# Optimization experiments

Measured on AMD Instinct MI355X. Metric: run time of the kernel, lower is better.

The kernel has to match this reference:

```python
import jax, jax.numpy as jnp
import numpy as np

BETA = 0.25  # commitment_weight


def _conv(x, w, b=None, stride=1, pad=0):
    y = jax.lax.conv_general_dilated(x, w, (stride, stride), ((pad, pad), (pad, pad)),
                                     dimension_numbers=('NCHW', 'OIHW', 'NCHW'))
    return y if b is None else y + b[None, :, None, None]


def _convT(x, w, b):
    # PyTorch ConvTranspose2d(kernel=4, stride=2, padding=1); w stored as (in, out, 4, 4)
    wf = jnp.flip(w, (2, 3)).transpose(1, 0, 2, 3)  # -> OIHW, spatially flipped
    y = jax.lax.conv_general_dilated(x, wf, (1, 1), ((2, 2), (2, 2)), lhs_dilation=(2, 2),
                                     dimension_numbers=('NCHW', 'OIHW', 'NCHW'))
    return y + b[None, :, None, None]


def _res(x, wa, wb):
    # ResidualLayer: x + conv1x1(relu(conv3x3(x))) , both convs bias-free
    return x + _conv(jax.nn.relu(_conv(x, wa, pad=1)), wb)


def _lrelu(x):
    return jax.nn.leaky_relu(x, 0.01)


def setup_inputs() -> dict:
    key = jax.random.key(0)
    ks = iter(jax.random.split(key, 32))
    def p(shape, s=0.05):
        return jax.random.normal(next(ks), shape, jnp.float32) * s
    inp = {
        'inputs': jax.random.normal(next(ks), (16, 4, 256, 256), jnp.float32),
        # encoder
        'e1_w': p((64, 4, 4, 4)),    'e1_b': p((64,)),
        'e2_w': p((128, 64, 4, 4)),  'e2_b': p((128,)),
        'e3_w': p((128, 128, 3, 3)), 'e3_b': p((128,)),
        'r1a_w': p((128, 128, 3, 3)), 'r1b_w': p((128, 128, 1, 1)),
        'r2a_w': p((128, 128, 3, 3)), 'r2b_w': p((128, 128, 1, 1)),
        'e4_w': p((64, 128, 1, 1)),  'e4_b': p((64,)),
        # residual VQ codebooks: (num_quantizers, codebook_size, dim)
        'codebooks': p((4, 512, 64), 1.0),
        # decoder
        'd1_w': p((128, 64, 3, 3)),  'd1_b': p((128,)),
        'dr1a_w': p((128, 128, 3, 3)), 'dr1b_w': p((128, 128, 1, 1)),
        'dr2a_w': p((128, 128, 3, 3)), 'dr2b_w': p((128, 128, 1, 1)),
        'dt1_w': p((128, 64, 4, 4)), 'dt1_b': p((64,)),  # (in, out, kH, kW) torch layout
        'dt2_w': p((64, 4, 4, 4)),   'dt2_b': p((4,)),
    }
    return inp


def reference(inputs, e1_w, e1_b, e2_w, e2_b, e3_w, e3_b, r1a_w, r1b_w, r2a_w, r2b_w,
              e4_w, e4_b, codebooks, d1_w, d1_b, dr1a_w, dr1b_w, dr2a_w, dr2b_w,
              dt1_w, dt1_b, dt2_w, dt2_b):
    # ---- encoder ----
    h = _lrelu(_conv(inputs, e1_w, e1_b, 2, 1))
    h = _lrelu(_conv(h, e2_w, e2_b, 2, 1))
    h = _lrelu(_conv(h, e3_w, e3_b, 1, 1))
    h = _res(h, r1a_w, r1b_w)
    h = _res(h, r2a_w, r2b_w)
    h = _lrelu(h)
    h = _lrelu(_conv(h, e4_w, e4_b, 1, 0))
    # ---- residual vector quantization ----
    z = h.transpose(0, 2, 3, 1)                     # B,H,W,D
    B, H, W, D = z.shape
    r = z.reshape(-1, D)                            # N,D tokens
    q_out = jnp.zeros_like(r)
    idx_list, losses = [], []
    for i in range(codebooks.shape[0]):
        cb = codebooks[i]                           # K,D
        d = (r * r).sum(-1, keepdims=True) - 2.0 * (r @ cb.T) + (cb * cb).sum(-1)
        idx = jnp.argmin(d, axis=-1)                # N
        q = cb[idx]                                 # N,D gather
        losses.append(BETA * jnp.mean((jax.lax.stop_gradient(q) - r) ** 2))
        q_st = r + jax.lax.stop_gradient(q - r)     # straight-through
        q_out = q_out + q_st
        r = r - jax.lax.stop_gradient(q)            # residual for next stage
        idx_list.append(idx)
    indices = jnp.stack(idx_list, -1).reshape(B, H, W, -1)   # B,H,W,Q
    losses = jnp.stack(losses)                                # (Q,)
    qz = q_out.reshape(B, H, W, D).transpose(0, 3, 1, 2)      # B,D,H,W
    # ---- decoder ----
    h = _lrelu(_conv(qz, d1_w, d1_b, 1, 1))
    h = _res(h, dr1a_w, dr1b_w)
    h = _res(h, dr2a_w, dr2b_w)
    h = _lrelu(h)
    h = _lrelu(_convT(h, dt1_w, dt1_b))
    recons = jax.nn.relu(_convT(h, dt2_w, dt2_b))
    return recons, indices, losses
```

## Files before the change

### kernel.cpp

```cpp
#include <hip/hip_runtime.h>
#include <cstddef>


template<int ACT> __device__ __forceinline__ float actf(float v) {
    if constexpr (ACT == 1) return v > 0.f ? v : 0.f;
    else if constexpr (ACT == 2) return v > 0.f ? v : 0.01f * v;
    else return v;
}
__device__ __forceinline__ float lrelu_in(float v) { return v > 0.f ? v : 0.01f * v; }

template<int CIN, int COUT, int K, int S, int P, int HIN, int WIN, int HOUT, int WOUT,
         int ICC, int NPY, int ACT, bool BIAS>
__launch_bounds__(256, (NPY >= 4 ? 2 : 4))
__global__ void conv_k(const float* __restrict__ in, const float* __restrict__ w,
                       const float* __restrict__ bias, float* __restrict__ out)
{
    constexpr int K2 = K * K;
    constexpr int NR = S * (NPY - 1) + K;
    constexpr int BH = 16 * NPY;
    __shared__ float sw[ICC * K2 * 16];
    const int tid = threadIdx.x;
    const int tx = tid & 15, ty = tid >> 4;
    constexpr int TW = WOUT / 16;
    const int bx = blockIdx.x % TW, by = blockIdx.x / TW;
    const int ox = bx * 16 + tx;
    const int oy0 = by * BH + ty * NPY;
    const int oc0 = blockIdx.y * 16;
    const int n = blockIdx.z;
    const int ix0 = ox * S - P, iy0 = oy0 * S - P;

    int ro[NR]; float mr[NR];
#pragma unroll
    for (int r = 0; r < NR; ++r) {
        const int iy = iy0 + r;
        const bool v = (iy >= 0) && (iy < HIN);
        ro[r] = v ? iy * WIN : 0;
        mr[r] = v ? 1.f : 0.f;
    }
    int co[K]; float mc[K];
#pragma unroll
    for (int c = 0; c < K; ++c) {
        const int ix = ix0 + c;
        const bool v = (ix >= 0) && (ix < WIN);
        co[c] = v ? ix : 0;
        mc[c] = v ? 1.f : 0.f;
    }

    float acc[NPY][16];
#pragma unroll
    for (int py = 0; py < NPY; ++py)
#pragma unroll
        for (int j = 0; j < 16; ++j) acc[py][j] = 0.f;

    for (int ic0 = 0; ic0 < CIN; ic0 += ICC) {
        __syncthreads();
        for (int t = tid; t < ICC * K2 * 16; t += 256) {
            int oc_l = t & 15, r = t >> 4, k = r % K2, ic_l = r / K2;
            sw[(ic_l * K2 + k) * 16 + oc_l] =
                w[((size_t)(oc0 + oc_l) * CIN + ic0 + ic_l) * K2 + k];
        }
        __syncthreads();
#pragma unroll 1
        for (int ic_l = 0; ic_l < ICC; ++ic_l) {
            const float* ip = in + (size_t)(n * CIN + ic0 + ic_l) * HIN * WIN;
            float patch[NR][K];
#pragma unroll
            for (int r = 0; r < NR; ++r)
#pragma unroll
                for (int c = 0; c < K; ++c)
                    patch[r][c] = ip[ro[r] + co[c]] * (mr[r] * mc[c]);
            const float* swp = &sw[ic_l * K2 * 16];
#pragma unroll
            for (int ky = 0; ky < K; ++ky) {
#pragma unroll
                for (int kx = 0; kx < K; ++kx) {
                    const float4* wp = (const float4*)&swp[(ky * K + kx) * 16];
                    float4 w0 = wp[0], w1 = wp[1], w2 = wp[2], w3 = wp[3];
#pragma unroll
                    for (int py = 0; py < NPY; ++py) {
                        const float v = patch[py * S + ky][kx];
                        acc[py][0]  = fmaf(w0.x, v, acc[py][0]);
                        acc[py][1]  = fmaf(w0.y, v, acc[py][1]);
                        acc[py][2]  = fmaf(w0.z, v, acc[py][2]);
                        acc[py][3]  = fmaf(w0.w, v, acc[py][3]);
                        acc[py][4]  = fmaf(w1.x, v, acc[py][4]);
                        acc[py][5]  = fmaf(w1.y, v, acc[py][5]);
                        acc[py][6]  = fmaf(w1.z, v, acc[py][6]);
                        acc[py][7]  = fmaf(w1.w, v, acc[py][7]);
                        acc[py][8]  = fmaf(w2.x, v, acc[py][8]);
                        acc[py][9]  = fmaf(w2.y, v, acc[py][9]);
                        acc[py][10] = fmaf(w2.z, v, acc[py][10]);
                        acc[py][11] = fmaf(w2.w, v, acc[py][11]);
                        acc[py][12] = fmaf(w3.x, v, acc[py][12]);
                        acc[py][13] = fmaf(w3.y, v, acc[py][13]);
                        acc[py][14] = fmaf(w3.z, v, acc[py][14]);
                        acc[py][15] = fmaf(w3.w, v, acc[py][15]);
                    }
                }
            }
        }
    }
#pragma unroll
    for (int py = 0; py < NPY; ++py) {
#pragma unroll
        for (int j = 0; j < 16; ++j) {
            float r = acc[py][j];
            if (BIAS) r += bias[oc0 + j];
            r = actf<ACT>(r);
            out[((size_t)(n * COUT + oc0 + j) * HOUT + oy0 + py) * WOUT + ox] = r;
        }
    }
}

template<int CIN, int COUT, int NPX, int ACT, bool BIAS, bool INL, bool RESID, bool TOK>
__launch_bounds__(256, 3)
__global__ void conv1x1_k(const float* __restrict__ in, const float* __restrict__ w,
                          const float* __restrict__ bias, const float* __restrict__ resid,
                          float* __restrict__ out)
{
    constexpr int HW = 4096;
    __shared__ float sw[16 * CIN];
    const int tid = threadIdx.x;
    const int base = blockIdx.x * (256 * NPX) + tid;
    const int oc0 = blockIdx.y * 16;
    const int n = blockIdx.z;

    for (int t = tid; t < 16 * CIN; t += 256) {
        int oc_l = t & 15, ic = t >> 4;
        sw[ic * 16 + oc_l] = w[(size_t)(oc0 + oc_l) * CIN + ic];
    }
    __syncthreads();

    float acc[NPX][16];
#pragma unroll
    for (int p = 0; p < NPX; ++p)
#pragma unroll
        for (int j = 0; j < 16; ++j) acc[p][j] = 0.f;

    const float* ip = in + (size_t)n * CIN * HW;
#pragma unroll 2
    for (int ic = 0; ic < CIN; ++ic) {
        float v[NPX];
#pragma unroll
        for (int p = 0; p < NPX; ++p) {
            float t = ip[(size_t)ic * HW + base + 256 * p];
            if (INL) t = lrelu_in(t);
            v[p] = t;
        }
        const float4* wp = (const float4*)&sw[ic * 16];
#pragma unroll
        for (int q4 = 0; q4 < 4; ++q4) {
            const float4 wv = wp[q4];
#pragma unroll
            for (int p = 0; p < NPX; ++p) {
                acc[p][q4 * 4 + 0] = fmaf(wv.x, v[p], acc[p][q4 * 4 + 0]);
                acc[p][q4 * 4 + 1] = fmaf(wv.y, v[p], acc[p][q4 * 4 + 1]);
                acc[p][q4 * 4 + 2] = fmaf(wv.z, v[p], acc[p][q4 * 4 + 2]);
                acc[p][q4 * 4 + 3] = fmaf(wv.w, v[p], acc[p][q4 * 4 + 3]);
            }
        }
    }
#pragma unroll
    for (int p = 0; p < NPX; ++p) {
        const int pix = base + 256 * p;
#pragma unroll
        for (int j = 0; j < 16; ++j) {
            float r = acc[p][j];
            if (BIAS) r += bias[oc0 + j];
            r = actf<ACT>(r);
            if (RESID) r += resid[((size_t)(n * COUT + oc0 + j)) * HW + pix];
            if (TOK)
                out[((size_t)n * HW + pix) * COUT + oc0 + j] = r;
            else
                out[((size_t)(n * COUT + oc0 + j)) * HW + pix] = r;
        }
    }
}

template<int CIN, int COUT, int OCT, int HIN, int ICC, int ACT, bool INL>
__launch_bounds__(256, 2)
__global__ void convt_k(const float* __restrict__ in, const float* __restrict__ w,
                        const float* __restrict__ bias, float* __restrict__ out)
{
    constexpr int WIN = HIN, HOUT = 2 * HIN, WOUT = 2 * HIN;
    __shared__ float sw[ICC * 16 * OCT];
    const int tid = threadIdx.x;
    const int tx = tid & 15, ty = tid >> 4;
    constexpr int TBW = WOUT / 32;
    const int bx = blockIdx.x % TBW, by = blockIdx.x / TBW;
    const int A0 = by * 32 + ty;
    const int A1 = A0 + 16;
    const int C = bx * 16 + tx;
    const int oc0 = blockIdx.y * OCT;
    const int n = blockIdx.z;

    int offs[2][9]; float msk[2][9];
#pragma unroll
    for (int h = 0; h < 2; ++h) {
        const int A = h ? A1 : A0;
#pragma unroll
        for (int dy = 0; dy < 3; ++dy) {
#pragma unroll
            for (int dx = 0; dx < 3; ++dx) {
                const int iy = A - 1 + dy, ix = C - 1 + dx;
                const bool v = (iy >= 0) && (iy < HIN) && (ix >= 0) && (ix < WIN);
                offs[h][dy * 3 + dx] = v ? iy * WIN + ix : 0;
                msk[h][dy * 3 + dx] = v ? 1.f : 0.f;
            }
        }
    }

    float acc[2][4 * OCT];
#pragma unroll
    for (int h = 0; h < 2; ++h)
#pragma unroll
        for (int j = 0; j < 4 * OCT; ++j) acc[h][j] = 0.f;

    for (int ic0 = 0; ic0 < CIN; ic0 += ICC) {
        __syncthreads();
        for (int t = tid; t < ICC * 16 * OCT; t += 256) {
            int oc_l = t % OCT, r = t / OCT, k = r & 15, ic_l = r >> 4;
            sw[(ic_l * 16 + k) * OCT + oc_l] =
                w[((size_t)(ic0 + ic_l) * COUT + oc0 + oc_l) * 16 + k];
        }
        __syncthreads();
#pragma unroll 1
        for (int ic_l = 0; ic_l < ICC; ++ic_l) {
            const float* ip = in + (size_t)(n * CIN + ic0 + ic_l) * HIN * WIN;
            float in9[2][9];
#pragma unroll
            for (int h = 0; h < 2; ++h)
#pragma unroll
                for (int j = 0; j < 9; ++j) {
                    float v = ip[offs[h][j]] * msk[h][j];
                    if (INL) v = lrelu_in(v);
                    in9[h][j] = v;
                }
#pragma unroll
            for (int ky = 0; ky < 4; ++ky) {
                const int ry = (ky + 1) & 1;
                const int dy = 2 - ((ky + 1) >> 1);
#pragma unroll
                for (int kx = 0; kx < 4; ++kx) {
                    const int rx = (kx + 1) & 1;
                    const int dx = 2 - ((kx + 1) >> 1);
                    const float va = in9[0][dy * 3 + dx];
                    const float vb = in9[1][dy * 3 + dx];
                    const int po = ry * 2 + rx;
                    const float4* wp = (const float4*)&sw[(ic_l * 16 + ky * 4 + kx) * OCT];
#pragma unroll
                    for (int q4 = 0; q4 < OCT / 4; ++q4) {
                        float4 wv = wp[q4];
                        acc[0][po * OCT + q4 * 4 + 0] = fmaf(wv.x, va, acc[0][po * OCT + q4 * 4 + 0]);
                        acc[0][po * OCT + q4 * 4 + 1] = fmaf(wv.y, va, acc[0][po * OCT + q4 * 4 + 1]);
                        acc[0][po * OCT + q4 * 4 + 2] = fmaf(wv.z, va, acc[0][po * OCT + q4 * 4 + 2]);
                        acc[0][po * OCT + q4 * 4 + 3] = fmaf(wv.w, va, acc[0][po * OCT + q4 * 4 + 3]);
                        acc[1][po * OCT + q4 * 4 + 0] = fmaf(wv.x, vb, acc[1][po * OCT + q4 * 4 + 0]);
                        acc[1][po * OCT + q4 * 4 + 1] = fmaf(wv.y, vb, acc[1][po * OCT + q4 * 4 + 1]);
                        acc[1][po * OCT + q4 * 4 + 2] = fmaf(wv.z, vb, acc[1][po * OCT + q4 * 4 + 2]);
                        acc[1][po * OCT + q4 * 4 + 3] = fmaf(wv.w, vb, acc[1][po * OCT + q4 * 4 + 3]);
                    }
                }
            }
        }
    }
#pragma unroll
    for (int h = 0; h < 2; ++h) {
        const int A = h ? A1 : A0;
#pragma unroll
        for (int po = 0; po < 4; ++po) {
            const int ry = po >> 1, rx = po & 1;
            const int oy = 2 * A + ry, ox = 2 * C + rx;
#pragma unroll
            for (int j = 0; j < OCT; ++j) {
                float r = acc[h][po * OCT + j] + bias[oc0 + j];
                r = actf<ACT>(r);
                out[((size_t)(n * COUT + oc0 + j) * HOUT + oy) * WOUT + ox] = r;
            }
        }
    }
}

__global__ void norm_k(const float* __restrict__ cb, float* __restrict__ nrm) {
    const int c = blockIdx.x * 256 + threadIdx.x;
    const float4* p = (const float4*)(cb + (size_t)c * 64);
    float a0 = 0.f, a1 = 0.f, a2 = 0.f, a3 = 0.f;
#pragma unroll
    for (int i = 0; i < 16; ++i) {
        float4 v = p[i];
        a0 = fmaf(v.x, v.x, a0); a1 = fmaf(v.y, v.y, a1);
        a2 = fmaf(v.z, v.z, a2); a3 = fmaf(v.w, v.w, a3);
    }
    nrm[c] = (a0 + a1) + (a2 + a3);
}

__launch_bounds__(256, 2)
__global__ void rvq_k(const float* __restrict__ z, const float* __restrict__ cb,
                      const float* __restrict__ nrm,
                      float* __restrict__ q, float* __restrict__ idx_out,
                      float* __restrict__ loss_acc)
{
    __shared__ float scb[256 * 64];
    __shared__ float snrm[256];
    __shared__ float lmin[4][2][64];
    __shared__ int   lidx[4][2][64];
    const int tid = threadIdx.x;
    const int lane = tid & 63;
    const int w = __builtin_amdgcn_readfirstlane(tid >> 6);
    const int t0 = blockIdx.x * 128 + lane;
    const int t1 = t0 + 64;

    float r0[64], r1[64];
    {
        const float4* zp0 = (const float4*)(z + (size_t)t0 * 64);
        const float4* zp1 = (const float4*)(z + (size_t)t1 * 64);
#pragma unroll
        for (int i = 0; i < 16; ++i) {
            float4 v = zp0[i];
            r0[4 * i + 0] = v.x; r0[4 * i + 1] = v.y;
            r0[4 * i + 2] = v.z; r0[4 * i + 3] = v.w;
            float4 u = zp1[i];
            r1[4 * i + 0] = u.x; r1[4 * i + 1] = u.y;
            r1[4 * i + 2] = u.z; r1[4 * i + 3] = u.w;
        }
    }

    for (int s = 0; s < 4; ++s) {
        float sr20, sr21;
        {
            float a0 = 0.f, a1 = 0.f, a2 = 0.f, a3 = 0.f;
            float b0 = 0.f, b1 = 0.f, b2 = 0.f, b3 = 0.f;
#pragma unroll
            for (int i = 0; i < 32; i += 4) {
                a0 = fmaf(r0[i + 0], r0[i + 0], a0);
                a1 = fmaf(r0[i + 1], r0[i + 1], a1);
                a2 = fmaf(r0[i + 2], r0[i + 2], a2);
                a3 = fmaf(r0[i + 3], r0[i + 3], a3);
                b0 = fmaf(r0[32 + i + 0], r0[32 + i + 0], b0);
                b1 = fmaf(r0[32 + i + 1], r0[32 + i + 1], b1);
                b2 = fmaf(r0[32 + i + 2], r0[32 + i + 2], b2);
                b3 = fmaf(r0[32 + i + 3], r0[32 + i + 3], b3);
            }
            sr20 = ((a0 + a1) + (a2 + a3)) + ((b0 + b1) + (b2 + b3));
        }
        {
            float a0 = 0.f, a1 = 0.f, a2 = 0.f, a3 = 0.f;
            float b0 = 0.f, b1 = 0.f, b2 = 0.f, b3 = 0.f;
#pragma unroll
            for (int i = 0; i < 32; i += 4) {
                a0 = fmaf(r1[i + 0], r1[i + 0], a0);
                a1 = fmaf(r1[i + 1], r1[i + 1], a1);
                a2 = fmaf(r1[i + 2], r1[i + 2], a2);
                a3 = fmaf(r1[i + 3], r1[i + 3], a3);
                b0 = fmaf(r1[32 + i + 0], r1[32 + i + 0], b0);
                b1 = fmaf(r1[32 + i + 1], r1[32 + i + 1], b1);
                b2 = fmaf(r1[32 + i + 2], r1[32 + i + 2], b2);
                b3 = fmaf(r1[32 + i + 3], r1[32 + i + 3], b3);
            }
            sr21 = ((a0 + a1) + (a2 + a3)) + ((b0 + b1) + (b2 + b3));
        }

        float dmin0 = 3.4e38f, dmin1 = 3.4e38f;
        int best0 = 0, best1 = 0;

        for (int pass = 0; pass < 2; ++pass) {
            __syncthreads();
            {
                const float4* csrc = (const float4*)(cb + (size_t)s * 512 * 64);
                for (int i = tid; i < 4096; i += 256) {
                    const int row = i >> 4, f4 = i & 15;
                    const int grow = (row >> 6) * 128 + pass * 64 + (row & 63);
                    ((float4*)scb)[row * 16 + f4] = csrc[(size_t)grow * 16 + f4];
                }
                const int g = (tid >> 6) * 128 + pass * 64 + (tid & 63);
                snrm[tid] = nrm[s * 512 + g];
            }
            __syncthreads();

#pragma unroll 2
            for (int kk = 0; kk < 64; ++kk) {
                const float4* cp = (const float4*)&scb[(size_t)(w * 64 + kk) * 64];
                float a0 = 0.f, a1 = 0.f, a2 = 0.f, a3 = 0.f;
                float e0 = 0.f, e1 = 0.f, e2 = 0.f, e3 = 0.f;
#pragma unroll
                for (int i = 0; i < 8; ++i) {
                    float4 c = cp[i];
                    a0 = fmaf(r0[4 * i + 0], c.x, a0);
                    a1 = fmaf(r0[4 * i + 1], c.y, a1);
                    a2 = fmaf(r0[4 * i + 2], c.z, a2);
                    a3 = fmaf(r0[4 * i + 3], c.w, a3);
                    e0 = fmaf(r1[4 * i + 0], c.x, e0);
                    e1 = fmaf(r1[4 * i + 1], c.y, e1);
                    e2 = fmaf(r1[4 * i + 2], c.z, e2);
                    e3 = fmaf(r1[4 * i + 3], c.w, e3);
                }
                float b0 = 0.f, b1 = 0.f, b2 = 0.f, b3 = 0.f;
                float f0 = 0.f, f1 = 0.f, f2 = 0.f, f3 = 0.f;
#pragma unroll
                for (int i = 0; i < 8; ++i) {
                    float4 c = cp[8 + i];
                    b0 = fmaf(r0[32 + 4 * i + 0], c.x, b0);
                    b1 = fmaf(r0[32 + 4 * i + 1], c.y, b1);
                    b2 = fmaf(r0[32 + 4 * i + 2], c.z, b2);
                    b3 = fmaf(r0[32 + 4 * i + 3], c.w, b3);
                    f0 = fmaf(r1[32 + 4 * i + 0], c.x, f0);
                    f1 = fmaf(r1[32 + 4 * i + 1], c.y, f1);
                    f2 = fmaf(r1[32 + 4 * i + 2], c.z, f2);
                    f3 = fmaf(r1[32 + 4 * i + 3], c.w, f3);
                }
                const float dot0 = ((a0 + a1) + (a2 + a3)) + ((b0 + b1) + (b2 + b3));
                const float dot1 = ((e0 + e1) + (e2 + e3)) + ((f0 + f1) + (f2 + f3));
                const float nk = snrm[w * 64 + kk];
                const float d0 = fmaf(-2.f, dot0, sr20) + nk;
                const float d1 = fmaf(-2.f, dot1, sr21) + nk;
                const int kl = pass * 64 + kk;
                if (d0 < dmin0) { dmin0 = d0; best0 = kl; }
                if (d1 < dmin1) { dmin1 = d1; best1 = kl; }
            }
        }

        lmin[w][0][lane] = dmin0; lidx[w][0][lane] = best0 + w * 128;
        lmin[w][1][lane] = dmin1; lidx[w][1][lane] = best1 + w * 128;
        __syncthreads();
        float d0c = lmin[0][0][lane]; int b0c = lidx[0][0][lane];
        float d1c = lmin[0][1][lane]; int b1c = lidx[0][1][lane];
#pragma unroll
        for (int ww = 1; ww < 4; ++ww) {
            const float dd0 = lmin[ww][0][lane]; const int ii0 = lidx[ww][0][lane];
            if (dd0 < d0c) { d0c = dd0; b0c = ii0; }
            const float dd1 = lmin[ww][1][lane]; const int ii1 = lidx[ww][1][lane];
            if (dd1 < d1c) { d1c = dd1; b1c = ii1; }
        }

        if (w < 2) {
            float lv = (w == 0) ? d0c : d1c;
#pragma unroll
            for (int off = 32; off; off >>= 1) lv += __shfl_down(lv, off, 64);
            if (lane == 0) atomicAdd(&loss_acc[s], lv);
        }
        if (w == 0)      idx_out[(size_t)t0 * 4 + s] = (float)b0c;
        else if (w == 1) idx_out[(size_t)t1 * 4 + s] = (float)b1c;

        const float4* c0 = (const float4*)(cb + ((size_t)s * 512 + b0c) * 64);
        const float4* c1 = (const float4*)(cb + ((size_t)s * 512 + b1c) * 64);
#pragma unroll
        for (int i = 0; i < 16; ++i) {
            float4 v = c0[i];
            r0[4 * i + 0] -= v.x; r0[4 * i + 1] -= v.y;
            r0[4 * i + 2] -= v.z; r0[4 * i + 3] -= v.w;
            float4 u = c1[i];
            r1[4 * i + 0] -= u.x; r1[4 * i + 1] -= u.y;
            r1[4 * i + 2] -= u.z; r1[4 * i + 3] -= u.w;
        }
    }

    if (w == 0) {
        const float4* zp = (const float4*)(z + (size_t)t0 * 64);
        const int n = t0 >> 12, pix = t0 & 4095;
        float* qp = q + (size_t)n * 64 * 4096 + pix;
#pragma unroll
        for (int i = 0; i < 16; ++i) {
            float4 v = zp[i];
            qp[(size_t)(4 * i + 0) * 4096] = v.x - r0[4 * i + 0];
            qp[(size_t)(4 * i + 1) * 4096] = v.y - r0[4 * i + 1];
            qp[(size_t)(4 * i + 2) * 4096] = v.z - r0[4 * i + 2];
            qp[(size_t)(4 * i + 3) * 4096] = v.w - r0[4 * i + 3];
        }
    } else if (w == 1) {
        const float4* zp = (const float4*)(z + (size_t)t1 * 64);
        const int n = t1 >> 12, pix = t1 & 4095;
        float* qp = q + (size_t)n * 64 * 4096 + pix;
#pragma unroll
        for (int i = 0; i < 16; ++i) {
            float4 v = zp[i];
            qp[(size_t)(4 * i + 0) * 4096] = v.x - r1[4 * i + 0];
            qp[(size_t)(4 * i + 1) * 4096] = v.y - r1[4 * i + 1];
            qp[(size_t)(4 * i + 2) * 4096] = v.z - r1[4 * i + 2];
            qp[(size_t)(4 * i + 3) * 4096] = v.w - r1[4 * i + 3];
        }
    }
}

__global__ void init_k(float* loss_acc) {
    if (threadIdx.x < 4) loss_acc[threadIdx.x] = 0.f;
}
__global__ void fin_k(const float* __restrict__ loss_acc, float* __restrict__ out_loss) {
    if (threadIdx.x < 4)
        out_loss[threadIdx.x] = loss_acc[threadIdx.x] * (0.25f / 4194304.f);
}

extern "C" void kernel_launch(void* const* d_in, const int* in_sizes, int n_in,
                              void* d_out, int out_size, void* d_ws, size_t ws_size,
                              hipStream_t stream)
{
    const float* x    = (const float*)d_in[0];
    const float* e1w  = (const float*)d_in[1];  const float* e1b = (const float*)d_in[2];
    const float* e2w  = (const float*)d_in[3];  const float* e2b = (const float*)d_in[4];
    const float* e3w  = (const float*)d_in[5];  const float* e3b = (const float*)d_in[6];
    const float* r1aw = (const float*)d_in[7];  const float* r1bw = (const float*)d_in[8];
    const float* r2aw = (const float*)d_in[9];  const float* r2bw = (const float*)d_in[10];
    const float* e4w  = (const float*)d_in[11]; const float* e4b = (const float*)d_in[12];
    const float* cbs  = (const float*)d_in[13];
    const float* d1w  = (const float*)d_in[14]; const float* d1b = (const float*)d_in[15];
    const float* dr1aw= (const float*)d_in[16]; const float* dr1bw = (const float*)d_in[17];
    const float* dr2aw= (const float*)d_in[18]; const float* dr2bw = (const float*)d_in[19];
    const float* dt1w = (const float*)d_in[20]; const float* dt1b = (const float*)d_in[21];
    const float* dt2w = (const float*)d_in[22]; const float* dt2b = (const float*)d_in[23];

    float* out = (float*)d_out;
    float* ws  = (float*)d_ws;

    float* BIG = ws;
    float* P2  = BIG;
    float* P3  = BIG + 8388608;
    float* P1  = ws + 16777216;
    float* Z   = ws + 25165824;
    float* Q   = ws + 29360128;
    float* LACC= ws + 33554432;
    float* NRM = ws + 33554448;

    float* out_recons = out;
    float* out_idx    = out + 4194304;
    float* out_loss   = out + 4194304 + 262144;

    init_k<<<1, 64, 0, stream>>>(LACC);
    norm_k<<<8, 256, 0, stream>>>(cbs, NRM);

    conv_k<4, 64, 4, 2, 1, 256, 256, 128, 128, 4, 2, 2, true>
        <<<dim3(32, 4, 16), 256, 0, stream>>>(x, e1w, e1b, BIG);
    conv_k<64, 128, 4, 2, 1, 128, 128, 64, 64, 16, 2, 2, true>
        <<<dim3(8, 8, 16), 256, 0, stream>>>(BIG, e2w, e2b, P1);
    conv_k<128, 128, 3, 1, 1, 64, 64, 64, 64, 16, 4, 2, true>
        <<<dim3(4, 8, 16), 256, 0, stream>>>(P1, e3w, e3b, P2);
    conv_k<128, 128, 3, 1, 1, 64, 64, 64, 64, 16, 4, 1, false>
        <<<dim3(4, 8, 16), 256, 0, stream>>>(P2, r1aw, nullptr, P3);
    conv1x1_k<128, 128, 4, 0, false, false, true, false>
        <<<dim3(4, 8, 16), 256, 0, stream>>>(P3, r1bw, nullptr, P2, P1);
    conv_k<128, 128, 3, 1, 1, 64, 64, 64, 64, 16, 4, 1, false>
        <<<dim3(4, 8, 16), 256, 0, stream>>>(P1, r2aw, nullptr, P3);
    conv1x1_k<128, 128, 4, 0, false, false, true, false>
        <<<dim3(4, 8, 16), 256, 0, stream>>>(P3, r2bw, nullptr, P1, P2);
    conv1x1_k<128, 64, 2, 2, true, true, false, true>
        <<<dim3(8, 4, 16), 256, 0, stream>>>(P2, e4w, e4b, nullptr, Z);

    rvq_k<<<512, 256, 0, stream>>>(Z, cbs, NRM, Q, out_idx, LACC);
    fin_k<<<1, 64, 0, stream>>>(LACC, out_loss);

    conv_k<64, 128, 3, 1, 1, 64, 64, 64, 64, 16, 4, 2, true>
        <<<dim3(4, 8, 16), 256, 0, stream>>>(Q, d1w, d1b, P1);
    conv_k<128, 128, 3, 1, 1, 64, 64, 64, 64, 16, 4, 1, false>
        <<<dim3(4, 8, 16), 256, 0, stream>>>(P1, dr1aw, nullptr, P2);
    conv1x1_k<128, 128, 4, 0, false, false, true, false>
        <<<dim3(4, 8, 16), 256, 0, stream>>>(P2, dr1bw, nullptr, P1, P3);
    conv_k<128, 128, 3, 1, 1, 64, 64, 64, 64, 16, 4, 1, false>
        <<<dim3(4, 8, 16), 256, 0, stream>>>(P3, dr2aw, nullptr, P2);
    conv1x1_k<128, 128, 4, 0, false, false, true, false>
        <<<dim3(4, 8, 16), 256, 0, stream>>>(P2, dr2bw, nullptr, P3, P1);
    convt_k<128, 64, 8, 64, 8, 2, true>
        <<<dim3(8, 8, 16), 256, 0, stream>>>(P1, dt1w, dt1b, BIG);
    convt_k<64, 4, 4, 128, 16, 1, false>
        <<<dim3(32, 1, 16), 256, 0, stream>>>(BIG, dt2w, dt2b, out_recons);
}
```

Before: 2.705 ms.

## Add specialized 3x3 stride-1 conv kernel with 8x8 register tile per thread

Adds a dedicated 3x3 same-padding conv kernel for the 64x64 feature maps. Each thread computes 8 output rows by 8 output channels and reads a 10x3 input patch straight from global memory per input channel, using precomputed row/column offsets and zero masks in place of branches. The block covers 32 columns by 64 rows, and weights for 8 output channels are staged in shared memory. All six 3x3 convolutions in the encoder and decoder now use it. The aim is better reuse of each input load and better occupancy than the generic conv kernel, at the cost of lower output-channel reuse per input load and more blocks along the channel axis.

```diff
diff --git a/kernel.cpp b/kernel.cpp
--- a/kernel.cpp
+++ b/kernel.cpp
@@ -112,6 +112,95 @@
     }
 }
 
+template<int CIN, int COUT, int ICC, int ACT, bool BIAS>
+__launch_bounds__(256, 2)
+__global__ void conv3_k(const float* __restrict__ in, const float* __restrict__ w,
+                        const float* __restrict__ bias, float* __restrict__ out)
+{
+    constexpr int HW = 64;
+    __shared__ float sw[ICC * 9 * 8];
+    const int tid = threadIdx.x;
+    const int tx = tid & 31, ty = tid >> 5;
+    const int ox = blockIdx.x * 32 + tx;
+    const int oy0 = ty * 8;
+    const int oc0 = blockIdx.y * 8;
+    const int n = blockIdx.z;
+
+    int ro[10]; float mr[10];
+#pragma unroll
+    for (int r = 0; r < 10; ++r) {
+        const int iy = oy0 - 1 + r;
+        const bool v = (iy >= 0) && (iy < HW);
+        ro[r] = v ? iy * HW : 0;
+        mr[r] = v ? 1.f : 0.f;
+    }
+    int co[3]; float mc[3];
+#pragma unroll
+    for (int c = 0; c < 3; ++c) {
+        const int ix = ox - 1 + c;
+        const bool v = (ix >= 0) && (ix < HW);
+        co[c] = v ? ix : 0;
+        mc[c] = v ? 1.f : 0.f;
+    }
+
+    float acc[8][8];
+#pragma unroll
+    for (int py = 0; py < 8; ++py)
+#pragma unroll
+        for (int j = 0; j < 8; ++j) acc[py][j] = 0.f;
+
+    for (int ic0 = 0; ic0 < CIN; ic0 += ICC) {
+        __syncthreads();
+        for (int t = tid; t < ICC * 9 * 8; t += 256) {
+            int oc_l = t & 7, r = t >> 3, k = r % 9, ic_l = r / 9;
+            sw[(ic_l * 9 + k) * 8 + oc_l] =
+                w[((size_t)(oc0 + oc_l) * CIN + ic0 + ic_l) * 9 + k];
+        }
+        __syncthreads();
+#pragma unroll 1
+        for (int ic_l = 0; ic_l < ICC; ++ic_l) {
+            const float* ip = in + (size_t)(n * CIN + ic0 + ic_l) * HW * HW;
+            float patch[10][3];
+#pragma unroll
+            for (int r = 0; r < 10; ++r)
+#pragma unroll
+                for (int c = 0; c < 3; ++c)
+                    patch[r][c] = ip[ro[r] + co[c]] * (mr[r] * mc[c]);
+            const float* swp = &sw[ic_l * 9 * 8];
+#pragma unroll
+            for (int ky = 0; ky < 3; ++ky) {
+#pragma unroll
+                for (int kx = 0; kx < 3; ++kx) {
+                    const float4* wp = (const float4*)&swp[(ky * 3 + kx) * 8];
+                    float4 w0 = wp[0], w1 = wp[1];
+#pragma unroll
+                    for (int py = 0; py < 8; ++py) {
+                        const float v = patch[py + ky][kx];
+                        acc[py][0] = fmaf(w0.x, v, acc[py][0]);
+                        acc[py][1] = fmaf(w0.y, v, acc[py][1]);
+                        acc[py][2] = fmaf(w0.z, v, acc[py][2]);
+                        acc[py][3] = fmaf(w0.w, v, acc[py][3]);
+                        acc[py][4] = fmaf(w1.x, v, acc[py][4]);
+                        acc[py][5] = fmaf(w1.y, v, acc[py][5]);
+                        acc[py][6] = fmaf(w1.z, v, acc[py][6]);
+                        acc[py][7] = fmaf(w1.w, v, acc[py][7]);
+                    }
+                }
+            }
+        }
+    }
+#pragma unroll
+    for (int py = 0; py < 8; ++py) {
+#pragma unroll
+        for (int j = 0; j < 8; ++j) {
+            float r = acc[py][j];
+            if (BIAS) r += bias[oc0 + j];
+            r = actf<ACT>(r);
+            out[((size_t)(n * COUT + oc0 + j) * HW + oy0 + py) * HW + ox] = r;
+        }
+    }
+}
+
 template<int CIN, int COUT, int NPX, int ACT, bool BIAS, bool INL, bool RESID, bool TOK>
 __launch_bounds__(256, 3)
 __global__ void conv1x1_k(const float* __restrict__ in, const float* __restrict__ w,
@@ -530,14 +619,14 @@
         <<<dim3(32, 4, 16), 256, 0, stream>>>(x, e1w, e1b, BIG);
     conv_k<64, 128, 4, 2, 1, 128, 128, 64, 64, 16, 2, 2, true>
         <<<dim3(8, 8, 16), 256, 0, stream>>>(BIG, e2w, e2b, P1);
-    conv_k<128, 128, 3, 1, 1, 64, 64, 64, 64, 16, 4, 2, true>
-        <<<dim3(4, 8, 16), 256, 0, stream>>>(P1, e3w, e3b, P2);
-    conv_k<128, 128, 3, 1, 1, 64, 64, 64, 64, 16, 4, 1, false>
-        <<<dim3(4, 8, 16), 256, 0, stream>>>(P2, r1aw, nullptr, P3);
+    conv3_k<128, 128, 16, 2, true>
+        <<<dim3(2, 16, 16), 256, 0, stream>>>(P1, e3w, e3b, P2);
+    conv3_k<128, 128, 16, 1, false>
+        <<<dim3(2, 16, 16), 256, 0, stream>>>(P2, r1aw, nullptr, P3);
     conv1x1_k<128, 128, 4, 0, false, false, true, false>
         <<<dim3(4, 8, 16), 256, 0, stream>>>(P3, r1bw, nullptr, P2, P1);
-    conv_k<128, 128, 3, 1, 1, 64, 64, 64, 64, 16, 4, 1, false>
-        <<<dim3(4, 8, 16), 256, 0, stream>>>(P1, r2aw, nullptr, P3);
+    conv3_k<128, 128, 16, 1, false>
+        <<<dim3(2, 16, 16), 256, 0, stream>>>(P1, r2aw, nullptr, P3);
     conv1x1_k<128, 128, 4, 0, false, false, true, false>
         <<<dim3(4, 8, 16), 256, 0, stream>>>(P3, r2bw, nullptr, P1, P2);
     conv1x1_k<128, 64, 2, 2, true, true, false, true>
@@ -546,14 +635,14 @@
     rvq_k<<<512, 256, 0, stream>>>(Z, cbs, NRM, Q, out_idx, LACC);
     fin_k<<<1, 64, 0, stream>>>(LACC, out_loss);
 
-    conv_k<64, 128, 3, 1, 1, 64, 64, 64, 64, 16, 4, 2, true>
-        <<<dim3(4, 8, 16), 256, 0, stream>>>(Q, d1w, d1b, P1);
-    conv_k<128, 128, 3, 1, 1, 64, 64, 64, 64, 16, 4, 1, false>
-        <<<dim3(4, 8, 16), 256, 0, stream>>>(P1, dr1aw, nullptr, P2);
+    conv3_k<64, 128, 16, 2, true>
+        <<<dim3(2, 16, 16), 256, 0, stream>>>(Q, d1w, d1b, P1);
+    conv3_k<128, 128, 16, 1, false>
+        <<<dim3(2, 16, 16), 256, 0, stream>>>(P1, dr1aw, nullptr, P2);
     conv1x1_k<128, 128, 4, 0, false, false, true, false>
         <<<dim3(4, 8, 16), 256, 0, stream>>>(P2, dr1bw, nullptr, P1, P3);
-    conv_k<128, 128, 3, 1, 1, 64, 64, 64, 64, 16, 4, 1, false>
-        <<<dim3(4, 8, 16), 256, 0, stream>>>(P3, dr2aw, nullptr, P2);
+    conv3_k<128, 128, 16, 1, false>
+        <<<dim3(2, 16, 16), 256, 0, stream>>>(P3, dr2aw, nullptr, P2);
     conv1x1_k<128, 128, 4, 0, false, false, true, false>
         <<<dim3(4, 8, 16), 256, 0, stream>>>(P2, dr2bw, nullptr, P3, P1);
     convt_k<128, 64, 8, 64, 8, 2, true>
```

Result: no change. 2.726 ms (+0.8%).
